# Performance work log

Measured on AMD Instinct MI355X. Metric: run time of the kernel, lower is better.

The kernel has to match this reference:

```python
import jax, jax.numpy as jnp
import numpy as np

LATENT = 2000
N_GROUPS = 10000  # loci_count // window_size
KERNEL = 20       # window_size * 2; per-group input length is 1 so out length == KERNEL
BATCH = 128
EPS = 1e-5
SLOPE = 0.1


def setup_inputs() -> dict:
    key = jax.random.key(0)
    k1, k2, k3, k4, k5 = jax.random.split(key, 5)
    return {
        "z": jax.random.normal(k1, (BATCH, LATENT), dtype=jnp.float32),
        "W_fc": jax.random.normal(k2, (N_GROUPS, LATENT), dtype=jnp.float32) * 0.02,
        "b_fc": jax.random.normal(k3, (N_GROUPS,), dtype=jnp.float32) * 0.02,
        "gamma": jnp.ones((N_GROUPS,), dtype=jnp.float32),
        "beta": jnp.zeros((N_GROUPS,), dtype=jnp.float32),
        "conv_w": jax.random.normal(k4, (N_GROUPS, KERNEL), dtype=jnp.float32) * 0.1,
        "conv_b": jax.random.normal(k5, (N_GROUPS,), dtype=jnp.float32) * 0.02,
    }


def reference(z, W_fc, b_fc, gamma, beta, conv_w, conv_b):
    # Linear: (B, L) @ (L, G) -> (B, G)
    h = jnp.einsum("bl,gl->bg", z, W_fc) + b_fc
    # BatchNorm1d (training mode: biased batch statistics, eps=1e-5)
    mean = jnp.mean(h, axis=0)
    var = jnp.mean(jnp.square(h - mean), axis=0)
    h = (h - mean) * jax.lax.rsqrt(var + EPS) * gamma + beta
    h = jnp.where(h >= 0, h, SLOPE * h)  # LeakyReLU(0.1)
    # Grouped ConvTranspose1d with per-group input length 1 degenerates to
    # an outer product per channel: y[b,g,k] = h[b,g]*w[g,k] + b[g]
    y = h[:, :, None] * conv_w[None, :, :] + conv_b[None, :, None]  # (B, G, K)
    y = jnp.where(y >= 0, y, SLOPE * y)  # LeakyReLU(0.1)
    out = jax.nn.sigmoid(y.reshape(z.shape[0], N_GROUPS * KERNEL))
    return out
```

## Files before the change

### kernel.cpp

```cpp
#include <hip/hip_runtime.h>
#include <hip/hip_bf16.h>
#include <stdint.h>

#define BATCH 128
#define LAT   2000
#define NG    10000
#define KW    20
#define OUTW  (NG * KW)
#define EPSV  1e-5f

#define NKT   32
#define EG    16
#define WROW  2048
#define HR_STRIDE 132

typedef __bf16 bf16x8 __attribute__((ext_vector_type(8)));
typedef float  f32x4  __attribute__((ext_vector_type(4)));

__device__ __forceinline__ ushort f2bf(float f) {
  uint32_t u = __builtin_bit_cast(uint32_t, f);
  u = (u + 0x7FFFu + ((u >> 16) & 1u)) >> 16;
  return (ushort)u;
}

__device__ __forceinline__ int4 pack8(const float* p) {
  float4 f0 = *(const float4*)p;
  float4 f1 = *(const float4*)(p + 4);
  int4 v;
  v.x = (int)((uint32_t)f2bf(f0.x) | ((uint32_t)f2bf(f0.y) << 16));
  v.y = (int)((uint32_t)f2bf(f0.z) | ((uint32_t)f2bf(f0.w) << 16));
  v.z = (int)((uint32_t)f2bf(f1.x) | ((uint32_t)f2bf(f1.y) << 16));
  v.w = (int)((uint32_t)f2bf(f1.z) | ((uint32_t)f2bf(f1.w) << 16));
  return v;
}

__global__ __launch_bounds__(256) void zprep_kernel(
    const float* __restrict__ zp, int4* __restrict__ zlin) {
  const int cg = blockIdx.x * 256 + threadIdx.x;
  const int r  = cg >> 8;
  const int ck = cg & 255;
  const int k0 = ck * 8;
  int4 v = make_int4(0, 0, 0, 0);
  if (k0 < LAT) v = pack8(zp + (size_t)r * LAT + k0);
  const int kt = ck >> 3, kk = (ck >> 2) & 1, q = ck & 3;
  const int dst = ((kt * 2 + kk) * 8 + (r >> 4)) * 64 + q * 16 + (r & 15);
  zlin[dst] = v;
}

__global__ __launch_bounds__(512, 2) void fused16_kernel(
    const int4* __restrict__ zlin, const float* __restrict__ wp,
    const float* __restrict__ gammap, const float* __restrict__ betap,
    const float* __restrict__ convwp, const float* __restrict__ convbp,
    float* __restrict__ out) {
  const int tid = threadIdx.x;
  const int g0  = blockIdx.x * EG;

  __shared__ __attribute__((aligned(16))) ushort Wl[EG * WROW];
  __shared__ float  h_raw[EG * HR_STRIDE];
  __shared__ float4 cw_s[EG * 5];
  __shared__ float  cb_s[EG];
  __shared__ float  scale_s[EG];
  __shared__ float  shift_s[EG];

  if (tid < EG * 5)
    cw_s[tid] = *(const float4*)(convwp + (size_t)g0 * KW + tid * 4);
  if (tid < EG) cb_s[tid] = convbp[g0 + tid];

#pragma unroll
  for (int i = 0; i < 8; ++i) {
    int cc  = i * 512 + tid;
    int row = cc >> 8;
    int c   = cc & 255;
    int kt  = c >> 3, j = c & 7;
    int k0  = kt * 64 + j * 8;
    int4 v  = make_int4(0, 0, 0, 0);
    if (k0 < LAT) v = pack8(wp + (size_t)(g0 + row) * LAT + k0);
    *(int4*)&Wl[row * WROW + kt * 64 + ((j ^ (row & 7)) << 3)] = v;
  }
  __syncthreads();

  const int lane = tid & 63;
  const int w    = tid >> 6;
  const int q    = lane >> 4;
  const int cl   = lane & 15;
  const int rb   = w * 16 + cl;

  const int4* zw  = zlin + (size_t)w * 64 + lane;
  const int aoff0 = cl * WROW + ((q       ^ (cl & 7)) << 3);
  const int aoff1 = cl * WROW + (((4 + q) ^ (cl & 7)) << 3);

  f32x4 acc = {0.f, 0.f, 0.f, 0.f};

#pragma unroll 4
  for (int kt = 0; kt < NKT; ++kt) {
    int4 z0 = zw[(size_t)(kt * 2 + 0) * 512];
    int4 z1 = zw[(size_t)(kt * 2 + 1) * 512];
    bf16x8 a0 = *(const bf16x8*)&Wl[aoff0 + kt * 64];
    bf16x8 a1 = *(const bf16x8*)&Wl[aoff1 + kt * 64];
    acc = __builtin_amdgcn_mfma_f32_16x16x32_bf16(
        a0, __builtin_bit_cast(bf16x8, z0), acc, 0, 0, 0);
    acc = __builtin_amdgcn_mfma_f32_16x16x32_bf16(
        a1, __builtin_bit_cast(bf16x8, z1), acc, 0, 0, 0);
  }

#pragma unroll
  for (int r = 0; r < 4; ++r)
    h_raw[(q * 4 + r) * HR_STRIDE + rb] = acc[r];
  __syncthreads();

  {
    const int gl = tid >> 5;
    const int bb = (tid & 31) * 4;
    const float4 a = *(const float4*)&h_raw[gl * HR_STRIDE + bb];
    float sm = a.x + a.y + a.z + a.w;
    float sq = a.x * a.x + a.y * a.y + a.z * a.z + a.w * a.w;
#pragma unroll
    for (int m = 1; m < 32; m <<= 1) {
      sm += __shfl_xor(sm, m);
      sq += __shfl_xor(sq, m);
    }
    if ((tid & 31) == 0) {
      float mean = sm * (1.f / 128.f);
      float var  = sq * (1.f / 128.f) - mean * mean;
      var = (var < 0.f) ? 0.f : var;
      float inv   = __builtin_amdgcn_rsqf(var + EPSV);
      float scale = inv * gammap[g0 + gl];
      scale_s[gl] = scale;
      shift_s[gl] = betap[g0 + gl] - mean * scale;
    }
  }
  __syncthreads();

  if (tid < 480) {
    const int col4 = tid % 80;
    const int r0   = tid / 80;
    const int gl   = col4 / 5;
    const float4 w4  = cw_s[col4];
    const float  cb  = cb_s[gl];
    const float  scl = scale_s[gl];
    const float  sft = shift_s[gl];
    const float* hsrc = &h_raw[gl * HR_STRIDE];
    float* obase = out + (size_t)g0 * KW + (size_t)col4 * 4;
    for (int j = 0; j < 22; ++j) {
      const int row = j * 6 + r0;
      if (row < BATCH) {
        float h = hsrc[row];
        h = fmaf(h, scl, sft);
        h = fmaxf(h, h * 0.1f);
        float y0 = fmaf(h, w4.x, cb);
        float y1 = fmaf(h, w4.y, cb);
        float y2 = fmaf(h, w4.z, cb);
        float y3 = fmaf(h, w4.w, cb);
        y0 = fmaxf(y0, y0 * 0.1f);
        y1 = fmaxf(y1, y1 * 0.1f);
        y2 = fmaxf(y2, y2 * 0.1f);
        y3 = fmaxf(y3, y3 * 0.1f);
        float4 ov;
        ov.x = __builtin_amdgcn_rcpf(1.f + exp2f(y0 * -1.44269504f));
        ov.y = __builtin_amdgcn_rcpf(1.f + exp2f(y1 * -1.44269504f));
        ov.z = __builtin_amdgcn_rcpf(1.f + exp2f(y2 * -1.44269504f));
        ov.w = __builtin_amdgcn_rcpf(1.f + exp2f(y3 * -1.44269504f));
        *(float4*)(obase + (size_t)row * OUTW) = ov;
      }
    }
  }
}

#define BKF 64
__global__ __launch_bounds__(256, 2) void fused_decoder_kernel(
    const float* __restrict__ zp, const float* __restrict__ wp,
    const float* __restrict__ gammap, const float* __restrict__ betap,
    const float* __restrict__ convwp, const float* __restrict__ convbp,
    float* __restrict__ out) {
  const int tid = threadIdx.x;
  const int g0  = blockIdx.x * 32;

  __shared__ ushort As[BATCH * BKF];
  __shared__ ushort Bs[32 * BKF];
  __shared__ float statS[2][2][16];
  __shared__ float statQ[2][2][16];

  const int lane = tid & 63;
  const int w    = tid >> 6;
  const int wm   = w & 1;
  const int wn   = w >> 1;
  const int q    = lane >> 4;
  const int cl   = lane & 15;

  f32x4 acc[4];
  const f32x4 vzero = {0.f, 0.f, 0.f, 0.f};
#pragma unroll
  for (int i = 0; i < 4; ++i) acc[i] = vzero;

  for (int it = 0; it < 32; ++it) {
    const int k0 = it * BKF;
    __syncthreads();
#pragma unroll
    for (int i = 0; i < 4; ++i) {
      int c = i * 256 + tid;
      int r = c >> 3, sc = c & 7;
      int gk = k0 + sc * 8;
      int4 v = make_int4(0, 0, 0, 0);
      if (gk < LAT) v = pack8(zp + (size_t)r * LAT + gk);
      *(int4*)&As[r * BKF + ((sc ^ (r & 7)) << 3)] = v;
    }
    {
      int r = tid >> 3, sc = tid & 7;
      int g  = g0 + r;
      int gk = k0 + sc * 8;
      int4 v = make_int4(0, 0, 0, 0);
      if (gk < LAT && g < NG) v = pack8(wp + (size_t)g * LAT + gk);
      *(int4*)&Bs[r * BKF + ((sc ^ (r & 7)) << 3)] = v;
    }
    __syncthreads();
#pragma unroll
    for (int kk = 0; kk < 2; ++kk) {
      int sc = kk * 4 + q;
      bf16x8 af[4], bfr;
#pragma unroll
      for (int mt = 0; mt < 4; ++mt) {
        int ra = wm * 64 + mt * 16 + cl;
        af[mt] = *(const bf16x8*)&As[ra * BKF + ((sc ^ (ra & 7)) << 3)];
      }
      {
        int rbx = wn * 16 + cl;
        bfr = *(const bf16x8*)&Bs[rbx * BKF + ((sc ^ (rbx & 7)) << 3)];
      }
#pragma unroll
      for (int mt = 0; mt < 4; ++mt)
        acc[mt] = __builtin_amdgcn_mfma_f32_16x16x32_bf16(af[mt], bfr,
                                                          acc[mt], 0, 0, 0);
    }
  }

  float s = 0.f, ss = 0.f;
#pragma unroll
  for (int mt = 0; mt < 4; ++mt)
#pragma unroll
    for (int r = 0; r < 4; ++r) {
      float v = acc[mt][r];
      s += v; ss += v * v;
    }
  s += __shfl_xor(s, 16); ss += __shfl_xor(ss, 16);
  s += __shfl_xor(s, 32); ss += __shfl_xor(ss, 32);
  if (q == 0) { statS[wm][wn][cl] = s; statQ[wm][wn][cl] = ss; }
  __syncthreads();

  const int gcol = g0 + wn * 16 + cl;
  const int gc   = (gcol < NG) ? gcol : (NG - 1);
  float S = statS[0][wn][cl] + statS[1][wn][cl];
  float Q = statQ[0][wn][cl] + statQ[1][wn][cl];
  float mean = S * (1.f / 128.f);
  float var  = Q * (1.f / 128.f) - mean * mean;
  var = (var < 0.f) ? 0.f : var;
  float inv = __builtin_amdgcn_rsqf(var + EPSV);
  float ga = gammap[gc], be = betap[gc], cb = convbp[gc];
  float wv[KW];
  {
    const float4* pw = (const float4*)(convwp + (size_t)gc * KW);
#pragma unroll
    for (int j = 0; j < 5; ++j) {
      float4 f = pw[j];
      wv[4 * j] = f.x; wv[4 * j + 1] = f.y;
      wv[4 * j + 2] = f.z; wv[4 * j + 3] = f.w;
    }
  }
  float scale = inv * ga;
  float shift = be - mean * scale;
  const bool ok = (gcol < NG);
#pragma unroll
  for (int mt = 0; mt < 4; ++mt) {
#pragma unroll
    for (int r = 0; r < 4; ++r) {
      float h = acc[mt][r] * scale + shift;
      h = fmaxf(h, h * 0.1f);
      int b = wm * 64 + mt * 16 + q * 4 + r;
      float4 ov[5];
#pragma unroll
      for (int j = 0; j < 5; ++j) {
        float y0 = h * wv[4 * j]     + cb;
        float y1 = h * wv[4 * j + 1] + cb;
        float y2 = h * wv[4 * j + 2] + cb;
        float y3 = h * wv[4 * j + 3] + cb;
        y0 = fmaxf(y0, y0 * 0.1f);
        y1 = fmaxf(y1, y1 * 0.1f);
        y2 = fmaxf(y2, y2 * 0.1f);
        y3 = fmaxf(y3, y3 * 0.1f);
        ov[j].x = __builtin_amdgcn_rcpf(1.f + exp2f(y0 * -1.44269504f));
        ov[j].y = __builtin_amdgcn_rcpf(1.f + exp2f(y1 * -1.44269504f));
        ov[j].z = __builtin_amdgcn_rcpf(1.f + exp2f(y2 * -1.44269504f));
        ov[j].w = __builtin_amdgcn_rcpf(1.f + exp2f(y3 * -1.44269504f));
      }
      if (ok) {
        float4* po = (float4*)(out + (size_t)b * OUTW + (size_t)gcol * KW);
#pragma unroll
        for (int j = 0; j < 5; ++j) po[j] = ov[j];
      }
    }
  }
}

extern "C" void kernel_launch(void* const* d_in, const int* in_sizes, int n_in,
                              void* d_out, int out_size, void* d_ws, size_t ws_size,
                              hipStream_t stream) {
  const float* z     = (const float*)d_in[0];
  const float* W     = (const float*)d_in[1];
  const float* gamma = (const float*)d_in[3];
  const float* beta  = (const float*)d_in[4];
  const float* convw = (const float*)d_in[5];
  const float* convb = (const float*)d_in[6];
  float* out = (float*)d_out;

  const size_t zlin_bytes = (size_t)BATCH * 256 * 16;

  if (ws_size >= zlin_bytes) {
    int4* zlin = (int4*)d_ws;
    zprep_kernel<<<128, 256, 0, stream>>>(z, zlin);
    fused16_kernel<<<NG / EG, 512, 0, stream>>>(zlin, W, gamma, beta,
                                                convw, convb, out);
  } else {
    fused_decoder_kernel<<<(NG + 31) / 32, 256, 0, stream>>>(
        z, W, gamma, beta, convw, convb, out);
  }
}
```

Before: 201.4 us.

## Stream fp32 W rows directly into MFMA operands with register prefetch, dropping LDS staging

Each wave now loads its 16 W rows straight from global memory as fp32, converts them to bf16 in registers and feeds the MFMA. The next k-tile is prefetched in software, with indices clamped at the tail; the padding is safe because z is zero-padded there. This removes the 64KB LDS tile, its block-wide barrier and the serialized fill phase, and raises the occupancy hint from 2 to 6 blocks per CU. The cost is that all 8 waves in a block re-read and re-convert the same W rows through the caches, which multiplies L1/L2 traffic and conversion work.

```diff
diff --git a/kernel.cpp b/kernel.cpp
--- a/kernel.cpp
+++ b/kernel.cpp
@@ -11,7 +11,6 @@
 
 #define NKT   32
 #define EG    16
-#define WROW  2048
 #define HR_STRIDE 132
 
 typedef __bf16 bf16x8 __attribute__((ext_vector_type(8)));
@@ -32,6 +31,13 @@
   v.z = (int)((uint32_t)f2bf(f1.x) | ((uint32_t)f2bf(f1.y) << 16));
   v.w = (int)((uint32_t)f2bf(f1.z) | ((uint32_t)f2bf(f1.w) << 16));
   return v;
+}
+
+__device__ __forceinline__ bf16x8 cvt8(float4 a, float4 b) {
+  bf16x8 r;
+  r[0] = (__bf16)a.x; r[1] = (__bf16)a.y; r[2] = (__bf16)a.z; r[3] = (__bf16)a.w;
+  r[4] = (__bf16)b.x; r[5] = (__bf16)b.y; r[6] = (__bf16)b.z; r[7] = (__bf16)b.w;
+  return r;
 }
 
 __global__ __launch_bounds__(256) void zprep_kernel(
@@ -47,7 +53,7 @@
   zlin[dst] = v;
 }
 
-__global__ __launch_bounds__(512, 2) void fused16_kernel(
+__global__ __launch_bounds__(512, 6) void fused16_kernel(
     const int4* __restrict__ zlin, const float* __restrict__ wp,
     const float* __restrict__ gammap, const float* __restrict__ betap,
     const float* __restrict__ convwp, const float* __restrict__ convbp,
@@ -55,7 +61,6 @@
   const int tid = threadIdx.x;
   const int g0  = blockIdx.x * EG;
 
-  __shared__ __attribute__((aligned(16))) ushort Wl[EG * WROW];
   __shared__ float  h_raw[EG * HR_STRIDE];
   __shared__ float4 cw_s[EG * 5];
   __shared__ float  cb_s[EG];
@@ -66,41 +71,46 @@
     cw_s[tid] = *(const float4*)(convwp + (size_t)g0 * KW + tid * 4);
   if (tid < EG) cb_s[tid] = convbp[g0 + tid];
 
-#pragma unroll
-  for (int i = 0; i < 8; ++i) {
-    int cc  = i * 512 + tid;
-    int row = cc >> 8;
-    int c   = cc & 255;
-    int kt  = c >> 3, j = c & 7;
-    int k0  = kt * 64 + j * 8;
-    int4 v  = make_int4(0, 0, 0, 0);
-    if (k0 < LAT) v = pack8(wp + (size_t)(g0 + row) * LAT + k0);
-    *(int4*)&Wl[row * WROW + kt * 64 + ((j ^ (row & 7)) << 3)] = v;
-  }
-  __syncthreads();
-
   const int lane = tid & 63;
   const int w    = tid >> 6;
   const int q    = lane >> 4;
   const int cl   = lane & 15;
   const int rb   = w * 16 + cl;
 
-  const int4* zw  = zlin + (size_t)w * 64 + lane;
-  const int aoff0 = cl * WROW + ((q       ^ (cl & 7)) << 3);
-  const int aoff1 = cl * WROW + (((4 + q) ^ (cl & 7)) << 3);
+  const float* wrow = wp + (size_t)(g0 + cl) * LAT;
+  const int4*  zw   = zlin + (size_t)w * 64 + lane;
+  const int kq = q * 8;
 
   f32x4 acc = {0.f, 0.f, 0.f, 0.f};
 
-#pragma unroll 4
+  float4 wa0 = *(const float4*)(wrow + kq);
+  float4 wa1 = *(const float4*)(wrow + kq + 4);
+  float4 wb0 = *(const float4*)(wrow + 32 + kq);
+  float4 wb1 = *(const float4*)(wrow + 32 + kq + 4);
+  int4 z0 = zw[0];
+  int4 z1 = zw[512];
+
+#pragma unroll 2
   for (int kt = 0; kt < NKT; ++kt) {
-    int4 z0 = zw[(size_t)(kt * 2 + 0) * 512];
-    int4 z1 = zw[(size_t)(kt * 2 + 1) * 512];
-    bf16x8 a0 = *(const bf16x8*)&Wl[aoff0 + kt * 64];
-    bf16x8 a1 = *(const bf16x8*)&Wl[aoff1 + kt * 64];
+    const int tn = (kt + 1 < NKT) ? (kt + 1) : 0;
+    int ka = tn * 64 + kq;
+    int kb = tn * 64 + 32 + kq;
+    ka = (ka > LAT - 8) ? (LAT - 8) : ka;
+    kb = (kb > LAT - 8) ? (LAT - 8) : kb;
+    float4 na0 = *(const float4*)(wrow + ka);
+    float4 na1 = *(const float4*)(wrow + ka + 4);
+    float4 nb0 = *(const float4*)(wrow + kb);
+    float4 nb1 = *(const float4*)(wrow + kb + 4);
+    int4 nz0 = zw[(size_t)(tn * 2 + 0) * 512];
+    int4 nz1 = zw[(size_t)(tn * 2 + 1) * 512];
+
     acc = __builtin_amdgcn_mfma_f32_16x16x32_bf16(
-        a0, __builtin_bit_cast(bf16x8, z0), acc, 0, 0, 0);
+        cvt8(wa0, wa1), __builtin_bit_cast(bf16x8, z0), acc, 0, 0, 0);
     acc = __builtin_amdgcn_mfma_f32_16x16x32_bf16(
-        a1, __builtin_bit_cast(bf16x8, z1), acc, 0, 0, 0);
+        cvt8(wb0, wb1), __builtin_bit_cast(bf16x8, z1), acc, 0, 0, 0);
+
+    wa0 = na0; wa1 = na1; wb0 = nb0; wb1 = nb1;
+    z0 = nz0; z1 = nz1;
   }
 
 #pragma unroll
```

Measured after the change: 251.4 us. 1.25x slower.

## Pad W tile rows instead of XOR swizzle and prefetch z fragments four steps ahead

Applied to the files above, without the earlier changes.

Replaces the XOR-swizzled LDS layout of the bf16 weight tile with a padded row stride of 2056 elements to avoid bank conflicts. It also issues the first four k-steps of z global loads before the barrier and keeps a four-deep register rotation so each iteration's z loads are in flight ahead of the MFMAs. The aim is to hide global load latency behind the weight staging and the matrix math. The cost is more registers, which may hurt occupancy at two blocks per CU, and slightly more LDS.

```diff
diff --git a/kernel.cpp b/kernel.cpp
--- a/kernel.cpp
+++ b/kernel.cpp
@@ -11,7 +11,7 @@
 
 #define NKT   32
 #define EG    16
-#define WROW  2048
+#define WPAD  2056
 #define HR_STRIDE 132
 
 typedef __bf16 bf16x8 __attribute__((ext_vector_type(8)));
@@ -55,7 +55,7 @@
   const int tid = threadIdx.x;
   const int g0  = blockIdx.x * EG;
 
-  __shared__ __attribute__((aligned(16))) ushort Wl[EG * WROW];
+  __shared__ __attribute__((aligned(16))) ushort Wl[EG * WPAD];
   __shared__ float  h_raw[EG * HR_STRIDE];
   __shared__ float4 cw_s[EG * 5];
   __shared__ float  cb_s[EG];
@@ -75,9 +75,8 @@
     int k0  = kt * 64 + j * 8;
     int4 v  = make_int4(0, 0, 0, 0);
     if (k0 < LAT) v = pack8(wp + (size_t)(g0 + row) * LAT + k0);
-    *(int4*)&Wl[row * WROW + kt * 64 + ((j ^ (row & 7)) << 3)] = v;
-  }
-  __syncthreads();
+    *(int4*)&Wl[row * WPAD + kt * 64 + j * 8] = v;
+  }
 
   const int lane = tid & 63;
   const int w    = tid >> 6;
@@ -85,22 +84,36 @@
   const int cl   = lane & 15;
   const int rb   = w * 16 + cl;
 
-  const int4* zw  = zlin + (size_t)w * 64 + lane;
-  const int aoff0 = cl * WROW + ((q       ^ (cl & 7)) << 3);
-  const int aoff1 = cl * WROW + (((4 + q) ^ (cl & 7)) << 3);
+  const int4* zw = zlin + (size_t)w * 64 + lane;
+  const ushort* wl = &Wl[cl * WPAD];
 
   f32x4 acc = {0.f, 0.f, 0.f, 0.f};
+
+  int4 za0 = zw[0],    za1 = zw[512];
+  int4 zb0 = zw[1024], zb1 = zw[1536];
+  int4 zc0 = zw[2048], zc1 = zw[2560];
+  int4 zd0 = zw[3072], zd1 = zw[3584];
+
+  __syncthreads();
 
 #pragma unroll 4
   for (int kt = 0; kt < NKT; ++kt) {
-    int4 z0 = zw[(size_t)(kt * 2 + 0) * 512];
-    int4 z1 = zw[(size_t)(kt * 2 + 1) * 512];
-    bf16x8 a0 = *(const bf16x8*)&Wl[aoff0 + kt * 64];
-    bf16x8 a1 = *(const bf16x8*)&Wl[aoff1 + kt * 64];
+    const int tp = (kt + 4 < NKT) ? (kt + 4) : kt;
+    int4 ne0 = zw[(size_t)(tp * 2 + 0) * 512];
+    int4 ne1 = zw[(size_t)(tp * 2 + 1) * 512];
+
+    bf16x8 a0 = *(const bf16x8*)&wl[kt * 64 + q * 8];
+    bf16x8 a1 = *(const bf16x8*)&wl[kt * 64 + (4 + q) * 8];
+
     acc = __builtin_amdgcn_mfma_f32_16x16x32_bf16(
-        a0, __builtin_bit_cast(bf16x8, z0), acc, 0, 0, 0);
+        a0, __builtin_bit_cast(bf16x8, za0), acc, 0, 0, 0);
     acc = __builtin_amdgcn_mfma_f32_16x16x32_bf16(
-        a1, __builtin_bit_cast(bf16x8, z1), acc, 0, 0, 0);
+        a1, __builtin_bit_cast(bf16x8, za1), acc, 0, 0, 0);
+
+    za0 = zb0; za1 = zb1;
+    zb0 = zc0; zb1 = zc1;
+    zc0 = zd0; zc1 = zd1;
+    zd0 = ne0; zd1 = ne1;
   }
 
 #pragma unroll
```

Result: no change. 198.7 us (-1.3%).
